# Optimization experiments

Measured on AMD Instinct MI355X. Metric: run time of the kernel, lower is better.

## Reference

```python
import jax, jax.numpy as jnp
import numpy as np

EPS = 1e-6
D = 512      # embedding_dim
M = 4        # n_modules
B = 4        # batch
S = 128      # seq_len
K = 32       # stack_size
STEPS = 16   # max_steps (ACT)
SCALE = D ** (-0.5)


def _clin(zr, zi, Wr, Wi, sub):
    # complex linear: (Wr + i Wi)(zr + i zi), torch Linear convention y = x @ W.T
    yr = jnp.einsum(sub, zr, Wr) - jnp.einsum(sub, zi, Wi)
    yi = jnp.einsum(sub, zi, Wr) + jnp.einsum(sub, zr, Wi)
    return yr, yi


def forward_fn(x_real, x_imag, Wl_r, Wl_i, Wq_r, Wq_i, Wk_r, Wk_i, Wv_r, Wv_i,
               ln_scale, ln_shift, mod_bias, gate_mask,
               score_w, score_b, conf_w, conf_b, halt_w, halt_b,
               ctrl_w, ctrl_b, st_score_w, st_score_b, st_conf_w, st_conf_b):
    mem0 = jnp.zeros((B, K, 2 * D), x_real.dtype)
    ptr0 = jnp.zeros((B, K), x_real.dtype).at[:, 0].set(1.0)
    acc0 = jnp.zeros((B, S, 2 * D), x_real.dtype)
    rem0 = jnp.ones((B,), x_real.dtype)

    def step(carry, _):
        sr, si, mem, ptr, acc, rem = carry
        # ComplexAttentionBlock (all M modules vectorized on axis m)
        cr = 0.5 * x_real + 0.5 * sr
        ci = 0.5 * x_imag + 0.5 * si
        zr, zi = _clin(cr, ci, Wl_r, Wl_i, 'bsd,mod->bmso')   # [B,M,S,D]
        # ComplexLayerNorm (magnitude LN, unbiased var as torch.var default)
        mag = jnp.sqrt(zr * zr + zi * zi) + EPS
        mean = mag.mean(-1, keepdims=True)
        var = mag.var(-1, keepdims=True, ddof=1)
        nm = (mag - mean) / jnp.sqrt(var + EPS)
        nm = nm * ln_scale[None, :, None, :] + ln_shift[None, :, None, :]
        ph = jnp.arctan2(zi, zr)
        zr = nm * jnp.cos(ph)
        zi = nm * jnp.sin(ph)
        # ModReLU
        nrm = jnp.sqrt(zr * zr + zi * zi) + EPS
        sc = jax.nn.relu(nrm + mod_bias[None, :, None, :]) / nrm
        zr = zr * sc
        zi = zi * sc
        # ComplexAttention over concatenated real/imag q,k
        sub = 'bmsd,mod->bmso'
        qr, qi = _clin(zr, zi, Wq_r, Wq_i, sub)
        kr, ki = _clin(zr, zi, Wk_r, Wk_i, sub)
        vr, vi = _clin(zr, zi, Wv_r, Wv_i, sub)
        qf = jnp.concatenate([qr, qi], -1)   # [B,M,S,2D]
        kf = jnp.concatenate([kr, ki], -1)
        attn = jax.nn.softmax(jnp.einsum('bmse,bmte->bmst', qf, kf) * SCALE, axis=-1)
        ar = jnp.einsum('bmst,bmtd->bmsd', attn, vr)
        ai = jnp.einsum('bmst,bmtd->bmsd', attn, vi)
        # SigmoidGatingMask
        g = jax.nn.sigmoid(gate_mask)[None, :, None, :]
        pr = ar * g
        pi = ai * g
        flat = jnp.concatenate([pr, pi], -1)  # [B,M,S,2D]
        score = jnp.einsum('bmse,me->bms', flat, score_w) + score_b[None, :, None]
        conf = jax.nn.sigmoid(jnp.einsum('bmse,me->bms', flat, conf_w) + conf_b[None, :, None])
        halt = jnp.einsum('bmse,me->bms', flat, halt_w) + halt_b[None, :, None]
        # DifferentiableStack on seq-pooled broadcast state
        flat_in = jnp.concatenate([sr.mean(1), si.mean(1)], -1)  # [B,2D]
        control = jax.nn.softmax(flat_in @ ctrl_w + ctrl_b, axis=-1)  # [B,3]
        push, pop, noop = control[:, 0:1], control[:, 1:2], control[:, 2:3]
        ptr_up = jnp.roll(ptr, 1, axis=1)
        ptr_dn = jnp.roll(ptr, -1, axis=1)
        new_ptr = push * ptr_up + pop * ptr_dn + noop * ptr
        new_ptr = new_ptr / (new_ptr.sum(1, keepdims=True) + EPS)
        wmask = push * ptr_up                                   # [B,K]
        new_mem = wmask[..., None] * flat_in[:, None, :] + mem * (1.0 - wmask[..., None])
        read = (new_mem * new_ptr[..., None]).sum(1)            # [B,2D]
        sp_r, sp_i = read[:, :D], read[:, D:]
        st_sc = read @ st_score_w + st_score_b[0]               # [B]
        st_cf = jax.nn.sigmoid(read @ st_conf_w + st_conf_b[0])
        # combine M block proposals + stack proposal via score*confidence softmax
        all_pr = jnp.concatenate([pr, jnp.broadcast_to(sp_r[:, None, None, :], (B, 1, S, D))], 1)
        all_pi = jnp.concatenate([pi, jnp.broadcast_to(sp_i[:, None, None, :], (B, 1, S, D))], 1)
        all_sc = jnp.concatenate([score, jnp.broadcast_to(st_sc[:, None, None], (B, 1, S))], 1)
        all_cf = jnp.concatenate([conf, jnp.broadcast_to(st_cf[:, None, None], (B, 1, S))], 1)
        w = jax.nn.softmax(all_sc * all_cf, axis=1)[..., None]  # [B,M+1,S,1]
        new_sr = (w * all_pr).sum(1)
        new_si = (w * all_pi).sum(1)
        # ACT halting accumulation
        p = jax.nn.sigmoid(halt).mean(axis=(1, 2))              # [B]
        acc = acc + (p * rem)[:, None, None] * jnp.concatenate([new_sr, new_si], -1)
        rem = rem * (1.0 - p)
        return (new_sr, new_si, new_mem, new_ptr, acc, rem), None

    carry, _ = jax.lax.scan(step, (x_real, x_imag, mem0, ptr0, acc0, rem0), None, length=STEPS)
    sr, si, _, _, acc, rem = carry
    # add ACT remainder weight on final state
    out = acc + rem[:, None, None] * jnp.concatenate([sr, si], -1)
    return out  # [B,S,2D] real/imag concat


def setup_inputs() -> dict:
    key = jax.random.key(0)
    ks = jax.random.split(key, 24)
    w = 1.0 / np.sqrt(D)
    h = 0.02
    inp = {
        'x_real': jax.random.normal(ks[0], (B, S, D), jnp.float32),
        'x_imag': jax.random.normal(ks[1], (B, S, D), jnp.float32),
        'Wl_r': jax.random.normal(ks[2], (M, D, D), jnp.float32) * w,
        'Wl_i': jax.random.normal(ks[3], (M, D, D), jnp.float32) * w,
        'Wq_r': jax.random.normal(ks[4], (M, D, D), jnp.float32) * w,
        'Wq_i': jax.random.normal(ks[5], (M, D, D), jnp.float32) * w,
        'Wk_r': jax.random.normal(ks[6], (M, D, D), jnp.float32) * w,
        'Wk_i': jax.random.normal(ks[7], (M, D, D), jnp.float32) * w,
        'Wv_r': jax.random.normal(ks[8], (M, D, D), jnp.float32) * w,
        'Wv_i': jax.random.normal(ks[9], (M, D, D), jnp.float32) * w,
        'ln_scale': jnp.ones((M, D), jnp.float32),
        'ln_shift': jnp.zeros((M, D), jnp.float32),
        'mod_bias': jnp.zeros((M, D), jnp.float32),
        'gate_mask': jnp.ones((M, D), jnp.float32),
        'score_w': jax.random.normal(ks[10], (M, 2 * D), jnp.float32) * h,
        'score_b': jnp.zeros((M,), jnp.float32),
        'conf_w': jax.random.normal(ks[11], (M, 2 * D), jnp.float32) * h,
        'conf_b': jnp.zeros((M,), jnp.float32),
        'halt_w': jax.random.normal(ks[12], (M, 2 * D), jnp.float32) * h,
        'halt_b': jnp.full((M,), -4.0, jnp.float32),  # nn.init.constant_(halt_head.bias, -4.0)
        'ctrl_w': jax.random.normal(ks[13], (2 * D, 3), jnp.float32) * h,
        'ctrl_b': jnp.zeros((3,), jnp.float32),
        'st_score_w': jax.random.normal(ks[14], (2 * D,), jnp.float32) * h,
        'st_score_b': jnp.zeros((1,), jnp.float32),
        'st_conf_w': jax.random.normal(ks[15], (2 * D,), jnp.float32) * h,
        'st_conf_b': jnp.zeros((1,), jnp.float32),
    }
    return inp


def reference(x_real, x_imag, Wl_r, Wl_i, Wq_r, Wq_i, Wk_r, Wk_i, Wv_r, Wv_i,
              ln_scale, ln_shift, mod_bias, gate_mask,
              score_w, score_b, conf_w, conf_b, halt_w, halt_b,
              ctrl_w, ctrl_b, st_score_w, st_score_b, st_conf_w, st_conf_b):
    return forward_fn(x_real, x_imag, Wl_r, Wl_i, Wq_r, Wq_i, Wk_r, Wk_i, Wv_r, Wv_i,
                      ln_scale, ln_shift, mod_bias, gate_mask,
                      score_w, score_b, conf_w, conf_b, halt_w, halt_b,
                      ctrl_w, ctrl_b, st_score_w, st_score_b, st_conf_w, st_conf_b)
```

## Files before the change

kernel.cpp:

```cpp
#include <hip/hip_runtime.h>

#define DD 512
#define MM 4
#define BB 4
#define SS 128
#define KK 32
#define NSTEPS 16
#define EPSF 1e-6f
#define SCALEF 0.04419417382415922f
#define BMSD (BB * MM * SS * DD)

typedef unsigned short u16;
typedef __bf16 bf16x8 __attribute__((ext_vector_type(8)));
typedef u16 u16x8 __attribute__((ext_vector_type(8)));
typedef float f32x16 __attribute__((ext_vector_type(16)));
typedef unsigned int u32x4 __attribute__((ext_vector_type(4)));

__device__ inline void split_bf16(float x, u16& h, u16& l) {
  __bf16 hb = (__bf16)x;
  float hf = (float)hb;
  __bf16 lb = (__bf16)(x - hf);
  h = __builtin_bit_cast(u16, hb);
  l = __builtin_bit_cast(u16, lb);
}
// ... 156 lines not shown
  int l31 = lane & 31, khalf = (lane >> 5) * 8;

  f32x16 accP, accN, accI;
  for (int i = 0; i < 16; i++) { accP[i] = 0.f; accN[i] = 0.f; accI[i] = 0.f; }

  int it20 = split;
  int seg0 = it20 >> 3, k00 = (it20 & 7) * 64;
  int aofs0 = (seg0 == 1) ? 512 : 0, wofs0 = (seg0 == 2) ? 512 : 0;
  u16x8 g0 = *(const u16x8*)&Ar[arow0 * 1024 + aofs0 + k00 + lk8];
  u16x8 g1 = *(const u16x8*)&Ar[arow1 * 1024 + aofs0 + k00 + lk8];
  u16x8 g2 = *(const u16x8*)&Ai[arow0 * 1024 + aofs0 + k00 + lk8];
  u16x8 g3 = *(const u16x8*)&Ai[arow1 * 1024 + aofs0 + k00 + lk8];
  u16x8 g4 = *(const u16x8*)&Wr[wrow0 * 1024 + wofs0 + k00 + lk8];
  u16x8 g5 = *(const u16x8*)&Wr[wrow1 * 1024 + wofs0 + k00 + lk8];
  u16x8 g6 = *(const u16x8*)&Wi[wrow0 * 1024 + wofs0 + k00 + lk8];
  u16x8 g7 = *(const u16x8*)&Wi[wrow1 * 1024 + wofs0 + k00 + lk8];

  for (int jt = 0; jt < 12; ++jt) {
    __syncthreads();
    *(u16x8*)&sAr[lrow][lk8] = g0;
    *(u16x8*)&sAr[lrow + 32][lk8] = g1;
    *(u16x8*)&sAi[lrow][lk8] = g2;
    *(u16x8*)&sAi[lrow + 32][lk8] = g3;
    *(u16x8*)&sWr[lrow][lk8] = g4;
    *(u16x8*)&sWr[lrow + 32][lk8] = g5;
    *(u16x8*)&sWi[lrow][lk8] = g6;
    *(u16x8*)&sWi[lrow + 32][lk8] = g7;
    u16x8 n0, n1, n2, n3, n4, n5, n6, n7;
    if (jt < 11) {
      int it2 = 2 * (jt + 1) + split, seg = it2 >> 3, k0 = (it2 & 7) * 64;
      int aofs = (seg == 1) ? 512 : 0, wofs = (seg == 2) ? 512 : 0;
      n0 = *(const u16x8*)&Ar[arow0 * 1024 + aofs + k0 + lk8];
      n1 = *(const u16x8*)&Ar[arow1 * 1024 + aofs + k0 + lk8];
      n2 = *(const u16x8*)&Ai[arow0 * 1024 + aofs + k0 + lk8];
      n3 = *(const u16x8*)&Ai[arow1 * 1024 + aofs + k0 + lk8];
      n4 = *(const u16x8*)&Wr[wrow0 * 1024 + wofs + k0 + lk8];
      n5 = *(const u16x8*)&Wr[wrow1 * 1024 + wofs + k0 + lk8];
      n6 = *(const u16x8*)&Wi[wrow0 * 1024 + wofs + k0 + lk8];
      n7 = *(const u16x8*)&Wi[wrow1 * 1024 + wofs + k0 + lk8];
    }
    __syncthreads();
#pragma unroll
    for (int kk = 0; kk < 64; kk += 16) {
      bf16x8 fAr = *(const bf16x8*)&sAr[wrow + l31][kk + khalf];
      bf16x8 fAi = *(const bf16x8*)&sAi[wrow + l31][kk + khalf];
      bf16x8 fWr = *(const bf16x8*)&sWr[wcol + l31][kk + khalf];
      bf16x8 fWi = *(const bf16x8*)&sWi[wcol + l31][kk + khalf];
      accP = __builtin_amdgcn_mfma_f32_32x32x16_bf16(fAr, fWr, accP, 0, 0, 0);
      accN = __builtin_amdgcn_mfma_f32_32x32x16_bf16(fAi, fWi, accN, 0, 0, 0);
      accI = __builtin_amdgcn_mfma_f32_32x32x16_bf16(fAi, fWr, accI, 0, 0, 0);
      accI = __builtin_amdgcn_mfma_f32_32x32x16_bf16(fAr, fWi, accI, 0, 0, 0);
    }
    if (jt < 11) {
      g0 = n0; g1 = n1; g2 = n2; g3 = n3; g4 = n4; g5 = n5; g6 = n6; g7 = n7;
    }
  }

  int o = o_blk + wcol + l31;
  size_t sofs = (size_t)split * BMSD;
#pragma unroll
  for (int reg = 0; reg < 16; reg++) {
    int r_in = (reg & 3) + 8 * (reg >> 2) + 4 * (lane >> 5);
    int gr = row_blk + wrow + r_in;
    int b = gr >> 7, s = gr & (SS - 1);
    size_t crow = (size_t)((b * MM + m) * SS + s);
    Cr[sofs + crow * DD + o] = accP[reg] - accN[reg];
    Ci[sofs + crow * DD + o] = accI[reg];
  }
}

__global__ __launch_bounds__(256) void k_gemm_g(
    const u16* __restrict__ Ar, const u16* __restrict__ Ai,
    const u16* __restrict__ Wr, const u16* __restrict__ Wi,
    float* __restrict__ Hr, float* __restrict__ Hi) {
  __shared__ u16 sAr[64][LSTR], sAi[64][LSTR], sWr[64][LSTR], sWi[64][LSTR];
  int m = blockIdx.z;
  int row_blk = blockIdx.y * 64, o_blk = blockIdx.x * 64;
  int tid = threadIdx.x;

  int lrow = tid >> 3, lk8 = (tid & 7) << 3;
  size_t arow0 = (size_t)(m * 512 + row_blk + lrow), arow1 = arow0 + 32;
  size_t wrow0 = (size_t)(m * 512 + o_blk + lrow), wrow1 = wrow0 + 32;

  int wave = tid >> 6, lane = tid & 63;
  int wrow = (wave >> 1) * 32, wcol = (wave & 1) * 32;
  int l31 = lane & 31, khalf = (lane >> 5) * 8;

  f32x16 accP, accN, accI;
  for (int i = 0; i < 16; i++) { accP[i] = 0.f; accN[i] = 0.f; accI[i] = 0.f; }

  u16x8 g0 = *(const u16x8*)&Ar[arow0 * 1024 + lk8];
  u16x8 g1 = *(const u16x8*)&Ar[arow1 * 1024 + lk8];
  u16x8 g2 = *(const u16x8*)&Ai[arow0 * 1024 + lk8];
  u16x8 g3 = *(const u16x8*)&Ai[arow1 * 1024 + lk8];
  u16x8 g4 = *(const u16x8*)&Wr[wrow0 * 1024 + lk8];
  u16x8 g5 = *(const u16x8*)&Wr[wrow1 * 1024 + lk8];
  u16x8 g6 = *(const u16x8*)&Wi[wrow0 * 1024 + lk8];
  u16x8 g7 = *(const u16x8*)&Wi[wrow1 * 1024 + lk8];

  for (int it = 0; it < 24; ++it) {
    __syncthreads();
    *(u16x8*)&sAr[lrow][lk8] = g0;
    *(u16x8*)&sAr[lrow + 32][lk8] = g1;
    *(u16x8*)&sAi[lrow][lk8] = g2;
    *(u16x8*)&sAi[lrow + 32][lk8] = g3;
    *(u16x8*)&sWr[lrow][lk8] = g4;
    *(u16x8*)&sWr[lrow + 32][lk8] = g5;
    *(u16x8*)&sWi[lrow][lk8] = g6;
    *(u16x8*)&sWi[lrow + 32][lk8] = g7;
    u16x8 n0, n1, n2, n3, n4, n5, n6, n7;
    if (it < 23) {
      int it2 = it + 1, seg = it2 >> 3, k0 = (it2 & 7) * 64;
      int aofs = (seg == 1) ? 512 : 0, wofs = (seg == 2) ? 512 : 0;
      n0 = *(const u16x8*)&Ar[arow0 * 1024 + aofs + k0 + lk8];
      n1 = *(const u16x8*)&Ar[arow1 * 1024 + aofs + k0 + lk8];
      n2 = *(const u16x8*)&Ai[arow0 * 1024 + aofs + k0 + lk8];
      n3 = *(const u16x8*)&Ai[arow1 * 1024 + aofs + k0 + lk8];
      n4 = *(const u16x8*)&Wr[wrow0 * 1024 + wofs + k0 + lk8];
      n5 = *(const u16x8*)&Wr[wrow1 * 1024 + wofs + k0 + lk8];
      n6 = *(const u16x8*)&Wi[wrow0 * 1024 + wofs + k0 + lk8];
      n7 = *(const u16x8*)&Wi[wrow1 * 1024 + wofs + k0 + lk8];
    }
    __syncthreads();
#pragma unroll
    for (int kk = 0; kk < 64; kk += 16) {
      bf16x8 fAr = *(const bf16x8*)&sAr[wrow + l31][kk + khalf];
      bf16x8 fAi = *(const bf16x8*)&sAi[wrow + l31][kk + khalf];
      bf16x8 fWr = *(const bf16x8*)&sWr[wcol + l31][kk + khalf];
      bf16x8 fWi = *(const bf16x8*)&sWi[wcol + l31][kk + khalf];
      u32x4 t = __builtin_bit_cast(u32x4, fAi) ^ 0x80008000u;
      bf16x8 nAi = __builtin_bit_cast(bf16x8, t);
      accP = __builtin_amdgcn_mfma_f32_32x32x16_bf16(fAr, fWr, accP, 0, 0, 0);
      accN = __builtin_amdgcn_mfma_f32_32x32x16_bf16(fAi, fWi, accN, 0, 0, 0);
      accI = __builtin_amdgcn_mfma_f32_32x32x16_bf16(fAr, fWi, accI, 0, 0, 0);
      accI = __builtin_amdgcn_mfma_f32_32x32x16_bf16(nAi, fWr, accI, 0, 0, 0);
    }
    if (it < 23) {
      g0 = n0; g1 = n1; g2 = n2; g3 = n3; g4 = n4; g5 = n5; g6 = n6; g7 = n7;
    }
  }

  int o = o_blk + wcol + l31;
#pragma unroll
  for (int reg = 0; reg < 16; reg++) {
    int r_in = (reg & 3) + 8 * (reg >> 2) + 4 * (lane >> 5);
    int gr = row_blk + wrow + r_in;
    size_t crow = (size_t)(m * 512 + gr);
    Hr[crow * DD + o] = accP[reg] + accN[reg];
    Hi[crow * DD + o] = accI[reg];
  }
}

__global__ __launch_bounds__(256) void k_gemm_qkv(
    const u16* __restrict__ Ar, const u16* __restrict__ Ai,
    const u16* __restrict__ wbf, size_t WSLOT,
    u16* __restrict__ qbr, u16* __restrict__ qbi,
    u16* __restrict__ vbr, u16* __restrict__ vbi) {
  __shared__ u16 sAr[64][LSTR], sAi[64][LSTR], sWr[64][LSTR], sWi[64][LSTR];
  int zid = blockIdx.x;
  int m = zid >> 1, w = zid & 1;
  int slot = (w == 0) ? 8 : 6;
  const u16* Wr = wbf + (size_t)slot * WSLOT;
  const u16* Wi = Wr + WSLOT;
  int row_blk = blockIdx.z * 64, o_blk = blockIdx.y * 64;
  int tid = threadIdx.x;

  int lrow = tid >> 3, lk8 = (tid & 7) << 3;
  int gr0 = row_blk + lrow, gr1 = gr0 + 32;
  size_t arow0 = (size_t)(((gr0 >> 7) * MM + m) * SS + (gr0 & (SS - 1)));
  size_t arow1 = (size_t)(((gr1 >> 7) * MM + m) * SS + (gr1 & (SS - 1)));
  size_t wrow0 = (size_t)m * DD + o_blk + lrow, wrow1 = wrow0 + 32;

  int wave = tid >> 6, lane = tid & 63;
  int wrow = (wave >> 1) * 32, wcol = (wave & 1) * 32;
  int l31 = lane & 31, khalf = (lane >> 5) * 8;

  f32x16 accP, accN, accI;
  for (int i = 0; i < 16; i++) { accP[i] = 0.f; accN[i] = 0.f; accI[i] = 0.f; }

  u16x8 g0 = *(const u16x8*)&Ar[arow0 * 1024 + lk8];
  u16x8 g1 = *(const u16x8*)&Ar[arow1 * 1024 + lk8];
  u16x8 g2 = *(const u16x8*)&Ai[arow0 * 1024 + lk8];
  u16x8 g3 = *(const u16x8*)&Ai[arow1 * 1024 + lk8];
  u16x8 g4 = *(const u16x8*)&Wr[wrow0 * 1024 + lk8];
  u16x8 g5 = *(const u16x8*)&Wr[wrow1 * 1024 + lk8];
  u16x8 g6 = *(const u16x8*)&Wi[wrow0 * 1024 + lk8];
  u16x8 g7 = *(const u16x8*)&Wi[wrow1 * 1024 + lk8];

  for (int it = 0; it < 24; ++it) {
    __syncthreads();
    *(u16x8*)&sAr[lrow][lk8] = g0;
    *(u16x8*)&sAr[lrow + 32][lk8] = g1;
    *(u16x8*)&sAi[lrow][lk8] = g2;
    *(u16x8*)&sAi[lrow + 32][lk8] = g3;
    *(u16x8*)&sWr[lrow][lk8] = g4;
    *(u16x8*)&sWr[lrow + 32][lk8] = g5;
    *(u16x8*)&sWi[lrow][lk8] = g6;
    *(u16x8*)&sWi[lrow + 32][lk8] = g7;
    u16x8 n0, n1, n2, n3, n4, n5, n6, n7;
    if (it < 23) {
      int it2 = it + 1, seg = it2 >> 3, k0 = (it2 & 7) * 64;
      int aofs = (seg == 1) ? 512 : 0, wofs = (seg == 2) ? 512 : 0;
      n0 = *(const u16x8*)&Ar[arow0 * 1024 + aofs + k0 + lk8];
      n1 = *(const u16x8*)&Ar[arow1 * 1024 + aofs + k0 + lk8];
      n2 = *(const u16x8*)&Ai[arow0 * 1024 + aofs + k0 + lk8];
      n3 = *(const u16x8*)&Ai[arow1 * 1024 + aofs + k0 + lk8];
      n4 = *(const u16x8*)&Wr[wrow0 * 1024 + wofs + k0 + lk8];
      n5 = *(const u16x8*)&Wr[wrow1 * 1024 + wofs + k0 + lk8];
      n6 = *(const u16x8*)&Wi[wrow0 * 1024 + wofs + k0 + lk8];
      n7 = *(const u16x8*)&Wi[wrow1 * 1024 + wofs + k0 + lk8];
    }
    __syncthreads();
#pragma unroll
    for (int kk = 0; kk < 64; kk += 16) {
      bf16x8 fAr = *(const bf16x8*)&sAr[wrow + l31][kk + khalf];
      bf16x8 fAi = *(const bf16x8*)&sAi[wrow + l31][kk + khalf];
      bf16x8 fWr = *(const bf16x8*)&sWr[wcol + l31][kk + khalf];
      bf16x8 fWi = *(const bf16x8*)&sWi[wcol + l31][kk + khalf];
      accP = __builtin_amdgcn_mfma_f32_32x32x16_bf16(fAr, fWr, accP, 0, 0, 0);
      accN = __builtin_amdgcn_mfma_f32_32x32x16_bf16(fAi, fWi, accN, 0, 0, 0);
      accI = __builtin_amdgcn_mfma_f32_32x32x16_bf16(fAi, fWr, accI, 0, 0, 0);
      accI = __builtin_amdgcn_mfma_f32_32x32x16_bf16(fAr, fWi, accI, 0, 0, 0);
    }
    if (it < 23) {
      g0 = n0; g1 = n1; g2 = n2; g3 = n3; g4 = n4; g5 = n5; g6 = n6; g7 = n7;
    }
  }

  u16* Cr = (w == 0) ? qbr : vbr;
  u16* Ci = (w == 0) ? qbi : vbi;
  int o = o_blk + wcol + l31;
#pragma unroll
  for (int reg = 0; reg < 16; reg++) {
    int r_in = (reg & 3) + 8 * (reg >> 2) + 4 * (lane >> 5);
    int gr = row_blk + wrow + r_in;
    int b = gr >> 7, s = gr & (SS - 1);
    size_t crow = (size_t)((b * MM + m) * SS + s);
    u16 h, l;
    split_bf16(accP[reg] - accN[reg], h, l);
    Cr[crow * 1024 + o] = h;
    Cr[crow * 1024 + 512 + o] = l;
    split_bf16(accI[reg], h, l);
    Ci[crow * 1024 + o] = h;
    Ci[crow * 1024 + 512 + o] = l;
  }
}

__global__ __launch_bounds__(256) void k_scores_sm(
    const u16* __restrict__ Q_r, const u16* __restrict__ Q_i,
    const u16* __restrict__ K_r, const u16* __restrict__ K_i,
    u16* __restrict__ Pb) {
  __shared__ __align__(16) char smem[55296];
  u16 (*sQr)[LSTR] = (u16(*)[LSTR])smem;
  u16 (*sQi)[LSTR] = (u16(*)[LSTR])(smem + 9216);
  u16 (*sKr)[LSTR] = (u16(*)[LSTR])(smem + 18432);
  u16 (*sKi)[LSTR] = (u16(*)[LSTR])(smem + 36864);
  float (*stile)[132] = (float(*)[132])smem;

  int bm = blockIdx.z;
  int s_blk = blockIdx.y * 64;
  int tid = threadIdx.x;
  int lrow = tid >> 3, lk8 = (tid & 7) << 3;
  size_t qrow0 = (size_t)(bm * SS + s_blk + lrow), qrow1 = qrow0 + 32;
  size_t krow = (size_t)(bm * SS + lrow);

  int wave = tid >> 6, lane = tid & 63;
  int srow_w = (wave & 1) * 32;
  int tcol_w = (wave >> 1) * 64;
  int l31 = lane & 31, khalf = (lane >> 5) * 8;

  f32x16 acc0, acc1;
  for (int i = 0; i < 16; i++) { acc0[i] = 0.f; acc1[i] = 0.f; }

  u16x8 pf[12];
  pf[0] = *(const u16x8*)&Q_r[qrow0 * 1024 + lk8];
  pf[1] = *(const u16x8*)&Q_r[qrow1 * 1024 + lk8];
  pf[2] = *(const u16x8*)&Q_i[qrow0 * 1024 + lk8];
  pf[3] = *(const u16x8*)&Q_i[qrow1 * 1024 + lk8];
#pragma unroll
  for (int q = 0; q < 4; q++) {
    pf[4 + q] = *(const u16x8*)&K_r[(krow + q * 32) * 1024 + lk8];
    pf[8 + q] = *(const u16x8*)&K_i[(krow + q * 32) * 1024 + lk8];
  }

  for (int it = 0; it < 24; ++it) {
    __syncthreads();
    *(u16x8*)&sQr[lrow][lk8] = pf[0];
    *(u16x8*)&sQr[lrow + 32][lk8] = pf[1];
    *(u16x8*)&sQi[lrow][lk8] = pf[2];
    *(u16x8*)&sQi[lrow + 32][lk8] = pf[3];
#pragma unroll
    for (int q = 0; q < 4; q++) {
      *(u16x8*)&sKr[lrow + q * 32][lk8] = pf[4 + q];
      *(u16x8*)&sKi[lrow + q * 32][lk8] = pf[8 + q];
    }
    u16x8 nf[12];
    if (it < 23) {
      int it2 = it + 1, seg = it2 >> 3, k0 = (it2 & 7) * 64;
      int qofs = (seg == 1) ? 512 : 0;
      int kofs = (seg == 2) ? 512 : 0;
      nf[0] = *(const u16x8*)&Q_r[qrow0 * 1024 + qofs + k0 + lk8];
      nf[1] = *(const u16x8*)&Q_r[qrow1 * 1024 + qofs + k0 + lk8];
      nf[2] = *(const u16x8*)&Q_i[qrow0 * 1024 + qofs + k0 + lk8];
      nf[3] = *(const u16x8*)&Q_i[qrow1 * 1024 + qofs + k0 + lk8];
#pragma unroll
      for (int q = 0; q < 4; q++) {
        nf[4 + q] = *(const u16x8*)&K_r[(krow + q * 32) * 1024 + kofs + k0 + lk8];
        nf[8 + q] = *(const u16x8*)&K_i[(krow + q * 32) * 1024 + kofs + k0 + lk8];
      }
    }
    __syncthreads();
#pragma unroll
    for (int kk = 0; kk < 64; kk += 16) {
      bf16x8 fQr = *(const bf16x8*)&sQr[srow_w + l31][kk + khalf];
      bf16x8 fQi = *(const bf16x8*)&sQi[srow_w + l31][kk + khalf];
      bf16x8 fKr0 = *(const bf16x8*)&sKr[tcol_w + l31][kk + khalf];
      bf16x8 fKr1 = *(const bf16x8*)&sKr[tcol_w + 32 + l31][kk + khalf];
      bf16x8 fKi0 = *(const bf16x8*)&sKi[tcol_w + l31][kk + khalf];
      bf16x8 fKi1 = *(const bf16x8*)&sKi[tcol_w + 32 + l31][kk + khalf];
      acc0 = __builtin_amdgcn_mfma_f32_32x32x16_bf16(fQr, fKr0, acc0, 0, 0, 0);
      acc0 = __builtin_amdgcn_mfma_f32_32x32x16_bf16(fQi, fKi0, acc0, 0, 0, 0);
      acc1 = __builtin_amdgcn_mfma_f32_32x32x16_bf16(fQr, fKr1, acc1, 0, 0, 0);
      acc1 = __builtin_amdgcn_mfma_f32_32x32x16_bf16(fQi, fKi1, acc1, 0, 0, 0);
    }
    if (it < 23) {
#pragma unroll
      for (int j = 0; j < 12; j++) pf[j] = nf[j];
    }
  }

  __syncthreads();
#pragma unroll
  for (int reg = 0; reg < 16; reg++) {
    int r = srow_w + (reg & 3) + 8 * (reg >> 2) + 4 * (lane >> 5);
    stile[r][tcol_w + l31] = acc0[reg] * SCALEF;
    stile[r][tcol_w + 32 + l31] = acc1[reg] * SCALEF;
  }
  __syncthreads();
  int row = tid >> 2;
  int quarter = tid & 3;
  float mx = -3.4e38f;
#pragma unroll
  for (int j = 0; j < 32; j++) mx = fmaxf(mx, stile[row][quarter * 32 + j]);
  mx = fmaxf(mx, __shfl_xor(mx, 1));
  mx = fmaxf(mx, __shfl_xor(mx, 2));
  float ev[32];
  float sum = 0.f;
#pragma unroll
  for (int j = 0; j < 32; j++) {
    ev[j] = expf(stile[row][quarter * 32 + j] - mx);
    sum += ev[j];
  }
  sum += __shfl_xor(sum, 1);
  sum += __shfl_xor(sum, 2);
  float inv = 1.f / sum;
  size_t prow = (size_t)(bm * SS + s_blk + row) * 256;
#pragma unroll
  for (int j = 0; j < 32; j++) {
    int c = quarter * 32 + j;
    u16 h, l;
    split_bf16(ev[j] * inv, h, l);
    Pb[prow + c] = h;
    Pb[prow + 128 + c] = l;
  }
}

__global__ __launch_bounds__(256) void k_pv(
    const u16* __restrict__ Pb, const u16* __restrict__ vbr, const u16* __restrict__ vbi,
    const float* __restrict__ gate_mask,
    const float* __restrict__ score_w, const float* __restrict__ conf_w,
    const float* __restrict__ halt_w,
    float* __restrict__ pr, float* __restrict__ pi,
    float* __restrict__ scorev, float* __restrict__ confv, float* __restrict__ haltv) {
  __shared__ u16 sP[64][LSTR], sVr[64][LSTR], sVi[64][LSTR];
  int bm = blockIdx.z;
  int m = bm & (MM - 1);
  int s_blk = blockIdx.y * 64;
  int o_blk = blockIdx.x * 64;
  int tid = threadIdx.x;
  int lrow = tid >> 3, lk8 = (tid & 7) << 3;
  size_t prow0 = (size_t)(bm * SS + s_blk + lrow), prow1 = prow0 + 32;

  int wave = tid >> 6, lane = tid & 63;
  int wrow = (wave >> 1) * 32;
  int wcol = (wave & 1) * 32;
  int l31 = lane & 31, khalf = (lane >> 5) * 8;

  f32x16 accR, accI;
  for (int i = 0; i < 16; i++) { accR[i] = 0.f; accI[i] = 0.f; }

  for (int it = 0; it < 6; ++it) {
    int seg = it >> 1, k0 = (it & 1) * 64;
    int pofs = (seg == 1) ? 128 : 0;
    int vofs = (seg == 2) ? 512 : 0;
    u16x8 p0 = *(const u16x8*)&Pb[prow0 * 256 + pofs + k0 + lk8];
    u16x8 p1 = *(const u16x8*)&Pb[prow1 * 256 + pofs + k0 + lk8];
    size_t vrow0 = (size_t)(bm * SS + k0 + lrow), vrow1 = vrow0 + 32;
    u16x8 v0 = *(const u16x8*)&vbr[vrow0 * 1024 + vofs + o_blk + lk8];
    u16x8 v1 = *(const u16x8*)&vbr[vrow1 * 1024 + vofs + o_blk + lk8];
    u16x8 w0 = *(const u16x8*)&vbi[vrow0 * 1024 + vofs + o_blk + lk8];
    u16x8 w1 = *(const u16x8*)&vbi[vrow1 * 1024 + vofs + o_blk + lk8];
    __syncthreads();
    *(u16x8*)&sP[lrow][lk8] = p0;
    *(u16x8*)&sP[lrow + 32][lk8] = p1;
    *(u16x8*)&sVr[lrow][lk8] = v0;
    *(u16x8*)&sVr[lrow + 32][lk8] = v1;
    *(u16x8*)&sVi[lrow][lk8] = w0;
    *(u16x8*)&sVi[lrow + 32][lk8] = w1;
    __syncthreads();
#pragma unroll
    for (int kk = 0; kk < 64; kk += 16) {
      bf16x8 fP = *(const bf16x8*)&sP[wrow + l31][kk + khalf];
      u16x8 ar, ai;
#pragma unroll
      for (int j = 0; j < 8; j++) {
        ar[j] = sVr[kk + khalf + j][wcol + l31];
        ai[j] = sVi[kk + khalf + j][wcol + l31];
      }
      accR = __builtin_amdgcn_mfma_f32_32x32x16_bf16(fP, __builtin_bit_cast(bf16x8, ar), accR, 0, 0, 0);
      accI = __builtin_amdgcn_mfma_f32_32x32x16_bf16(fP, __builtin_bit_cast(bf16x8, ai), accI, 0, 0, 0);
    }
  }

  int d = o_blk + wcol + l31;
  float g = 1.f / (1.f + expf(-gate_mask[m * DD + d]));
  float swr = score_w[m * 2 * DD + d], swi = score_w[m * 2 * DD + DD + d];
  float cwr = conf_w[m * 2 * DD + d],  cwi = conf_w[m * 2 * DD + DD + d];
  float hwr = halt_w[m * 2 * DD + d],  hwi = halt_w[m * 2 * DD + DD + d];
#pragma unroll
  for (int reg = 0; reg < 16; reg++) {
    int r_in = (reg & 3) + 8 * (reg >> 2) + 4 * (lane >> 5);
    size_t crow = (size_t)(bm * SS + s_blk + wrow + r_in);
    float vR = accR[reg] * g, vI = accI[reg] * g;
    pr[crow * DD + d] = vR;
    pi[crow * DD + d] = vI;
    float ps = vR * swr + vI * swi;
    float pc = vR * cwr + vI * cwi;
    float ph = vR * hwr + vI * hwi;
#pragma unroll
    for (int off = 1; off < 32; off <<= 1) {
      ps += __shfl_xor(ps, off);
      pc += __shfl_xor(pc, off);
      ph += __shfl_xor(ph, off);
    }
    if (l31 == 0) {
      atomicAdd(&scorev[crow], ps);
      atomicAdd(&confv[crow], pc);
      atomicAdd(&haltv[crow], ph);
    }
  }
}

__global__ void k_lnphase(const float* __restrict__ zr, const float* __restrict__ zi,
                          const float* __restrict__ ln_scale, const float* __restrict__ ln_shift,
                          const float* __restrict__ mod_bias,
                          u16* __restrict__ zbr, u16* __restrict__ zbi) {
  int row = blockIdx.x;
  int m = (row >> 7) & (MM - 1);
  int tid = threadIdx.x;
  size_t base = (size_t)row * DD;
  float zrv[4], ziv[4], rv[4];
  float sum = 0.f, sumsq = 0.f;
#pragma unroll
  for (int i = 0; i < 4; i++) {
    int o = tid + i * 128;
    float a = zr[base + o] + zr[(size_t)BMSD + base + o];
    float bv = zi[base + o] + zi[(size_t)BMSD + base + o];
    zrv[i] = a; ziv[i] = bv;
    float r = sqrtf(a * a + bv * bv);
    rv[i] = r;
    float mg = r + EPSF;
    sum += mg;
    sumsq += mg * mg;
  }
  __shared__ float rs[128], rq[128];
  rs[tid] = sum; rq[tid] = sumsq;
  __syncthreads();
  for (int off = 64; off > 0; off >>= 1) {
    if (tid < off) { rs[tid] += rs[tid + off]; rq[tid] += rq[tid + off]; }
    __syncthreads();
  }
  float mean = rs[0] * (1.0f / DD);
  float var = (rq[0] - (float)DD * mean * mean) * (1.0f / (DD - 1));
  float inv = 1.0f / sqrtf(var + EPSF);
#pragma unroll
  for (int i = 0; i < 4; i++) {
    int o = tid + i * 128;
    float mg = rv[i] + EPSF;
    float nm = (mg - mean) * inv * ln_scale[m * DD + o] + ln_shift[m * DD + o];
    float r = rv[i];
    float cosp, sinp;
    if (r > 0.f) { cosp = zrv[i] / r; sinp = ziv[i] / r; }
    else { cosp = 1.f; sinp = 0.f; }
    float z1r = nm * cosp, z1i = nm * sinp;
    float nrm = sqrtf(z1r * z1r + z1i * z1i) + EPSF;
    float sc = fmaxf(nrm + mod_bias[m * DD + o], 0.f) / nrm;
    u16 h, l;
    split_bf16(z1r * sc, h, l);
    zbr[(size_t)row * 1024 + o] = h;
    zbr[(size_t)row * 1024 + 512 + o] = l;
    split_bf16(z1i * sc, h, l);
    zbi[(size_t)row * 1024 + o] = h;
    zbi[(size_t)row * 1024 + 512 + o] = l;
  }
}

__global__ void k_memup(const float* __restrict__ flat_in,
                        const float* __restrict__ nptrg, const float* __restrict__ wmg,
                        float* __restrict__ memv, float* __restrict__ readv,
                        const float* __restrict__ st_score_w, const float* __restrict__ st_conf_w,
                        float* __restrict__ stacc) {
  int b = blockIdx.x >> 2;
  int chunk = blockIdx.x & 3;
  int tid = threadIdx.x;
  int e = chunk * 256 + tid;
  __shared__ float nptr[KK], wm[KK];
  __shared__ float red[256], red2[256];
  if (tid < KK) { nptr[tid] = nptrg[b * KK + tid]; wm[tid] = wmg[b * KK + tid]; }
  __syncthreads();
  float fl = flat_in[b * 2 * DD + e];
  float racc = 0.f;
#pragma unroll
  for (int k = 0; k < KK; k++) {
    size_t idx = ((size_t)(b * KK + k)) * 2 * DD + e;
    float nm = wm[k] * fl + memv[idx] * (1.f - wm[k]);
    memv[idx] = nm;
    racc += nm * nptr[k];
  }
  readv[b * 2 * DD + e] = racc;
  red[tid] = racc * st_score_w[e];
  red2[tid] = racc * st_conf_w[e];
  __syncthreads();
  for (int off = 128; off > 0; off >>= 1) {
    if (tid < off) { red[tid] += red[tid + off]; red2[tid] += red2[tid + off]; }
    __syncthreads();
  }
  if (tid == 0) {
    atomicAdd(&stacc[b * 2], red[0]);
    atomicAdd(&stacc[b * 2 + 1], red2[0]);
  }
}

__global__ void k_haltp(const float* __restrict__ halt, const float* __restrict__ halt_b,
                        float* __restrict__ rem,
                        float* __restrict__ coeff, const float* __restrict__ stacc,
                        const float* __restrict__ st_score_b, const float* __restrict__ st_conf_b,
                        float* __restrict__ stv) {
  int b = blockIdx.x;
  int tid = threadIdx.x;
  __shared__ float red[256];
  float v0 = halt[b * MM * SS + tid] + halt_b[tid >> 7];
  float v1 = halt[b * MM * SS + 256 + tid] + halt_b[(tid + 256) >> 7];
  red[tid] = 1.f / (1.f + expf(-v0)) + 1.f / (1.f + expf(-v1));
  __syncthreads();
  for (int off = 128; off > 0; off >>= 1) {
    if (tid < off) red[tid] += red[tid + off];
    __syncthreads();
  }
  if (tid == 0) {
    float p = red[0] * (1.0f / (MM * SS));
    float r = rem[b];
    coeff[b] = p * r;
    rem[b] = r * (1.f - p);
    stv[b] = stacc[b * 2] + st_score_b[0];
    stv[BB + b] = 1.f / (1.f + expf(-(stacc[b * 2 + 1] + st_conf_b[0])));
  }
}

__global__ void k_combine(const float* __restrict__ pr, const float* __restrict__ pi,
                          const float* __restrict__ score, const float* __restrict__ conf,
                          const float* __restrict__ score_b, const float* __restrict__ conf_b,
                          const float* __restrict__ stv, const float* __restrict__ readv,
                          const float* __restrict__ coeff,
                          const float* __restrict__ xr, const float* __restrict__ xi,
                          float* __restrict__ sr, float* __restrict__ si, float* __restrict__ acc,
                          u16* __restrict__ crbf, u16* __restrict__ cibf) {
  int bs = blockIdx.x;
  int b = bs >> 7, s = bs & (SS - 1);
  int tid = threadIdx.x;
  __shared__ float w[5];
  if (tid == 0) {
    float l[5];
    for (int m = 0; m < MM; m++) {
      int r = (b * MM + m) * SS + s;
      float sc = score[r] + score_b[m];
      float cf = 1.f / (1.f + expf(-(conf[r] + conf_b[m])));
      l[m] = sc * cf;
    }
    l[4] = stv[b] * stv[BB + b];
    float mx = l[0];
    for (int j = 1; j < 5; j++) mx = fmaxf(mx, l[j]);
    float sum = 0.f;
    for (int j = 0; j < 5; j++) { l[j] = expf(l[j] - mx); sum += l[j]; }
    for (int j = 0; j < 5; j++) w[j] = l[j] / sum;
  }
  __syncthreads();
  float cf = coeff[b];
#pragma unroll
  for (int i = 0; i < 2; i++) {
    int d = tid + i * 256;
    float nsr = w[4] * readv[b * 2 * DD + d];
    float nsi = w[4] * readv[b * 2 * DD + DD + d];
#pragma unroll
    for (int m = 0; m < MM; m++) {
      size_t off = ((size_t)((b * MM + m) * SS + s)) * DD + d;
      nsr += w[m] * pr[off];
      nsi += w[m] * pi[off];
    }
    size_t sidx = (size_t)bs * DD + d;
    sr[sidx] = nsr;
    si[sidx] = nsi;
    size_t aoff = (size_t)bs * 2 * DD;
    acc[aoff + d] += cf * nsr;
    acc[aoff + DD + d] += cf * nsi;
    u16 h, l;
    split_bf16(0.5f * xr[sidx] + 0.5f * nsr, h, l);
    crbf[(size_t)bs * 1024 + d] = h;
    crbf[(size_t)bs * 1024 + 512 + d] = l;
    split_bf16(0.5f * xi[sidx] + 0.5f * nsi, h, l);
    cibf[(size_t)bs * 1024 + d] = h;
    cibf[(size_t)bs * 1024 + 512 + d] = l;
  }
}

__global__ void k_final(const float* __restrict__ acc, const float* __restrict__ rem,
                        const float* __restrict__ sr, const float* __restrict__ si,
                        float* __restrict__ out) {
  int idx = blockIdx.x * 256 + threadIdx.x;
  int e = idx & (2 * DD - 1);
  int bs = idx >> 10;
  int b = bs >> 7;
  float v = (e < DD) ? sr[(size_t)bs * DD + e] : si[(size_t)bs * DD + e - DD];
  out[idx] = acc[idx] + rem[b] * v;
}

extern "C" void kernel_launch(void* const* d_in, const int* in_sizes, int n_in,
                              void* d_out, int out_size, void* d_ws, size_t ws_size,
                              hipStream_t stream) {
  const float* xr = (const float*)d_in[0];
  const float* xi = (const float*)d_in[1];
  const float* Wl_r = (const float*)d_in[2];
  const float* Wl_i = (const float*)d_in[3];
  const float* Wq_r = (const float*)d_in[4];
  const float* Wq_i = (const float*)d_in[5];
  const float* Wk_r = (const float*)d_in[6];
  const float* Wk_i = (const float*)d_in[7];
  const float* Wv_r = (const float*)d_in[8];
  const float* Wv_i = (const float*)d_in[9];
  const float* ln_scale = (const float*)d_in[10];
  const float* ln_shift = (const float*)d_in[11];
  const float* mod_bias = (const float*)d_in[12];
  const float* gate_mask = (const float*)d_in[13];
  const float* score_w = (const float*)d_in[14];
  const float* score_b = (const float*)d_in[15];
  const float* conf_w = (const float*)d_in[16];
  const float* conf_b = (const float*)d_in[17];
  const float* halt_w = (const float*)d_in[18];
  const float* halt_b = (const float*)d_in[19];
  const float* ctrl_w = (const float*)d_in[20];
  const float* ctrl_b = (const float*)d_in[21];
  const float* st_score_w = (const float*)d_in[22];
  const float* st_score_b = (const float*)d_in[23];
  const float* st_conf_w = (const float*)d_in[24];
  const float* st_conf_b = (const float*)d_in[25];
  float* out = (float*)d_out;

  const int BSD = BB * SS * DD;
  const size_t WSLOT = (size_t)MM * DD * 1024;

  char* pc = (char*)d_ws;
  float* sr = (float*)pc; pc += (size_t)BSD * 4;
  float* si = (float*)pc; pc += (size_t)BSD * 4;
  float* zr = (float*)pc; pc += (size_t)2 * BMSD * 4;
  float* zi = (float*)pc; pc += (size_t)2 * BMSD * 4;
  float* prb = (float*)pc; pc += (size_t)BMSD * 4;
  float* pib = (float*)pc; pc += (size_t)BMSD * 4;
  float* scorev = (float*)pc; pc += (size_t)BB * MM * SS * 4;
  float* confv = (float*)pc; pc += (size_t)BB * MM * SS * 4;
  float* haltv = (float*)pc; pc += (size_t)BB * MM * SS * 4;
  float* flat = (float*)pc; pc += (size_t)BB * 2 * DD * 4;
  float* stacc = (float*)pc; pc += 64;
  float* nptrg = (float*)pc; pc += (size_t)BB * KK * 4;
  float* wmg = (float*)pc; pc += (size_t)BB * KK * 4;
  float* memv = (float*)pc; pc += (size_t)BB * KK * 2 * DD * 4;
  float* ptrv = (float*)pc; pc += (size_t)BB * KK * 4;
  float* readv = (float*)pc; pc += (size_t)BB * 2 * DD * 4;
  float* stv = (float*)pc; pc += (size_t)2 * BB * 4;
  float* accb = (float*)pc; pc += (size_t)BB * SS * 2 * DD * 4;
  float* rem = (float*)pc; pc += (size_t)BB * 4;
  float* coeff = (float*)pc; pc += (size_t)BB * 4;
  u16* crbf = (u16*)pc; pc += (size_t)BB * SS * 1024 * 2;
  u16* cibf = (u16*)pc; pc += (size_t)BB * SS * 1024 * 2;
  u16* zbr = (u16*)pc; pc += (size_t)BB * MM * SS * 1024 * 2;
  u16* zbi = (u16*)pc; pc += (size_t)BB * MM * SS * 1024 * 2;
  u16* qbr = (u16*)pc; pc += (size_t)BB * MM * SS * 1024 * 2;
  u16* qbi = (u16*)pc; pc += (size_t)BB * MM * SS * 1024 * 2;
  u16* vbr = (u16*)pc; pc += (size_t)BB * MM * SS * 1024 * 2;
  u16* vbi = (u16*)pc; pc += (size_t)BB * MM * SS * 1024 * 2;
  u16* Pb  = (u16*)pc; pc += (size_t)BB * MM * SS * 256 * 2;
  u16* wbf = (u16*)pc; pc += 10 * WSLOT * 2;
  u16* wqtr = (u16*)pc; pc += WSLOT * 2;
  u16* wqti = (u16*)pc; pc += WSLOT * 2;
  u16* wktr = (u16*)pc; pc += WSLOT * 2;
  u16* wkti = (u16*)pc; pc += WSLOT * 2;
  float* hfr = (float*)pc; pc += (size_t)MM * DD * DD * 4;
  float* hfi = (float*)pc; pc += (size_t)MM * DD * DD * 4;

  k_convw<<<4096, 256, 0, stream>>>(Wl_r, wbf + 0 * WSLOT);
  k_convw<<<4096, 256, 0, stream>>>(Wl_i, wbf + 1 * WSLOT);
  k_convw<<<4096, 256, 0, stream>>>(Wv_r, wbf + 6 * WSLOT);
  k_convw<<<4096, 256, 0, stream>>>(Wv_i, wbf + 7 * WSLOT);

  dim3 tgrid(8, 8, 4);
  k_convt<<<tgrid, 256, 0, stream>>>(Wq_r, wqtr);
  k_convt<<<tgrid, 256, 0, stream>>>(Wq_i, wqti);
  k_convt<<<tgrid, 256, 0, stream>>>(Wk_r, wktr);
  k_convt<<<tgrid, 256, 0, stream>>>(Wk_i, wkti);

  dim3 hgrid(8, 8, 4);
  k_gemm_g<<<hgrid, 256, 0, stream>>>(wktr, wkti, wqtr, wqti, hfr, hfi);
  k_convw<<<4096, 256, 0, stream>>>(hfr, wbf + 8 * WSLOT);
  k_convw<<<4096, 256, 0, stream>>>(hfi, wbf + 9 * WSLOT);

  k_init<<<2048, 256, 0, stream>>>(xr, xi, sr, si, accb, memv, ptrv, rem, crbf, cibf);

  dim3 ggrid(DD / 64, (BB * SS) / 64, MM * 2);
  dim3 qgrid(MM * 2, DD / 64, (BB * SS) / 64);
  dim3 smgrid(1, SS / 64, BB * MM);
  dim3 pvgrid(DD / 64, SS / 64, BB * MM);

  for (int step = 0; step < NSTEPS; ++step) {
    k_flatctrl<<<BB, 256, 0, stream>>>(sr, si, ctrl_w, ctrl_b, ptrv, flat, nptrg, wmg, stacc,
                                       scorev, confv, haltv);
    k_gemm_mfma<<<ggrid, 256, 0, stream>>>(crbf, cibf, wbf + 0 * WSLOT, wbf + 1 * WSLOT, zr, zi);
    k_lnphase<<<BB * MM * SS, 128, 0, stream>>>(zr, zi, ln_scale, ln_shift, mod_bias, zbr, zbi);
    k_gemm_qkv<<<qgrid, 256, 0, stream>>>(zbr, zbi, wbf, WSLOT, qbr, qbi, vbr, vbi);
    k_scores_sm<<<smgrid, 256, 0, stream>>>(qbr, qbi, zbr, zbi, Pb);
    k_pv<<<pvgrid, 256, 0, stream>>>(Pb, vbr, vbi, gate_mask, score_w, conf_w, halt_w,
                                     prb, pib, scorev, confv, haltv);
    k_memup<<<BB * 4, 256, 0, stream>>>(flat, nptrg, wmg, memv, readv,
                                        st_score_w, st_conf_w, stacc);
    k_haltp<<<BB, 256, 0, stream>>>(haltv, halt_b, rem, coeff, stacc, st_score_b, st_conf_b, stv);
    k_combine<<<BB * SS, 256, 0, stream>>>(prb, pib, scorev, confv, score_b, conf_b,
                                           stv, readv, coeff,
                                           xr, xi, sr, si, accb, crbf, cibf);
  }

  k_final<<<(BB * SS * 2 * DD) / 256, 256, 0, stream>>>(accb, rem, sr, si, out);
}
```

Measured before the change: 2.121 ms.

## Store V transposed from QKV GEMM so PV kernel reads contiguous MFMA fragments

The V projection inside the QKV GEMM now computes the transposed product by swapping operands (weights as A, activations as B) and writes V in a [b,m,d,s] layout with hi/lo bf16 halves along s. The PV kernel then loads V rows along the sequence dimension and reads MFMA B fragments with single vector LDS loads, replacing the per-element strided gather from shared memory. This removes LDS bank-conflicting scalar reads in PV, at the cost of narrower, strided global stores in the V epilogue.

```diff
diff --git a/kernel.cpp b/kernel.cpp
--- a/kernel.cpp
+++ b/kernel.cpp
@@ -332,40 +332,49 @@
 }
 
 __global__ __launch_bounds__(256) void k_gemm_qkv(
-    const u16* __restrict__ Ar, const u16* __restrict__ Ai,
+    const u16* __restrict__ Az_r, const u16* __restrict__ Az_i,
     const u16* __restrict__ wbf, size_t WSLOT,
     u16* __restrict__ qbr, u16* __restrict__ qbi,
-    u16* __restrict__ vbr, u16* __restrict__ vbi) {
+    u16* __restrict__ vbtr, u16* __restrict__ vbti) {
   __shared__ u16 sAr[64][LSTR], sAi[64][LSTR], sWr[64][LSTR], sWi[64][LSTR];
   int zid = blockIdx.x;
   int m = zid >> 1, w = zid & 1;
-  int slot = (w == 0) ? 8 : 6;
-  const u16* Wr = wbf + (size_t)slot * WSLOT;
-  const u16* Wi = Wr + WSLOT;
-  int row_blk = blockIdx.z * 64, o_blk = blockIdx.y * 64;
-  int tid = threadIdx.x;
-
+  int tid = threadIdx.x;
   int lrow = tid >> 3, lk8 = (tid & 7) << 3;
-  int gr0 = row_blk + lrow, gr1 = gr0 + 32;
-  size_t arow0 = (size_t)(((gr0 >> 7) * MM + m) * SS + (gr0 & (SS - 1)));
-  size_t arow1 = (size_t)(((gr1 >> 7) * MM + m) * SS + (gr1 & (SS - 1)));
-  size_t wrow0 = (size_t)m * DD + o_blk + lrow, wrow1 = wrow0 + 32;
-
   int wave = tid >> 6, lane = tid & 63;
   int wrow = (wave >> 1) * 32, wcol = (wave & 1) * 32;
   int l31 = lane & 31, khalf = (lane >> 5) * 8;
 
+  const u16 *Ar, *Ai, *Wr, *Wi;
+  size_t ra0, ra1, rw0, rw1;
+  if (w == 0) {
+    Ar = Az_r; Ai = Az_i;
+    Wr = wbf + (size_t)8 * WSLOT; Wi = wbf + (size_t)9 * WSLOT;
+    int row_blk = blockIdx.z * 64, o_blk = blockIdx.y * 64;
+    int gr0 = row_blk + lrow, gr1 = gr0 + 32;
+    ra0 = (size_t)(((gr0 >> 7) * MM + m) * SS + (gr0 & (SS - 1)));
+    ra1 = (size_t)(((gr1 >> 7) * MM + m) * SS + (gr1 & (SS - 1)));
+    rw0 = (size_t)m * DD + o_blk + lrow; rw1 = rw0 + 32;
+  } else {
+    Ar = wbf + (size_t)6 * WSLOT; Ai = wbf + (size_t)7 * WSLOT;
+    Wr = Az_r; Wi = Az_i;
+    int d_blk = blockIdx.y * 64;
+    int b = blockIdx.z >> 1, s0 = (blockIdx.z & 1) * 64;
+    ra0 = (size_t)m * DD + d_blk + lrow; ra1 = ra0 + 32;
+    rw0 = (size_t)((b * MM + m) * SS) + s0 + lrow; rw1 = rw0 + 32;
+  }
+
   f32x16 accP, accN, accI;
   for (int i = 0; i < 16; i++) { accP[i] = 0.f; accN[i] = 0.f; accI[i] = 0.f; }
 
-  u16x8 g0 = *(const u16x8*)&Ar[arow0 * 1024 + lk8];
-  u16x8 g1 = *(const u16x8*)&Ar[arow1 * 1024 + lk8];
-  u16x8 g2 = *(const u16x8*)&Ai[arow0 * 1024 + lk8];
-  u16x8 g3 = *(const u16x8*)&Ai[arow1 * 1024 + lk8];
-  u16x8 g4 = *(const u16x8*)&Wr[wrow0 * 1024 + lk8];
-  u16x8 g5 = *(const u16x8*)&Wr[wrow1 * 1024 + lk8];
-  u16x8 g6 = *(const u16x8*)&Wi[wrow0 * 1024 + lk8];
-  u16x8 g7 = *(const u16x8*)&Wi[wrow1 * 1024 + lk8];
+  u16x8 g0 = *(const u16x8*)&Ar[ra0 * 1024 + lk8];
+  u16x8 g1 = *(const u16x8*)&Ar[ra1 * 1024 + lk8];
+  u16x8 g2 = *(const u16x8*)&Ai[ra0 * 1024 + lk8];
+  u16x8 g3 = *(const u16x8*)&Ai[ra1 * 1024 + lk8];
+  u16x8 g4 = *(const u16x8*)&Wr[rw0 * 1024 + lk8];
+  u16x8 g5 = *(const u16x8*)&Wr[rw1 * 1024 + lk8];
+  u16x8 g6 = *(const u16x8*)&Wi[rw0 * 1024 + lk8];
+  u16x8 g7 = *(const u16x8*)&Wi[rw1 * 1024 + lk8];
 
   for (int it = 0; it < 24; ++it) {
     __syncthreads();
@@ -381,14 +390,14 @@
     if (it < 23) {
       int it2 = it + 1, seg = it2 >> 3, k0 = (it2 & 7) * 64;
       int aofs = (seg == 1) ? 512 : 0, wofs = (seg == 2) ? 512 : 0;
-      n0 = *(const u16x8*)&Ar[arow0 * 1024 + aofs + k0 + lk8];
-      n1 = *(const u16x8*)&Ar[arow1 * 1024 + aofs + k0 + lk8];
-      n2 = *(const u16x8*)&Ai[arow0 * 1024 + aofs + k0 + lk8];
-      n3 = *(const u16x8*)&Ai[arow1 * 1024 + aofs + k0 + lk8];
-      n4 = *(const u16x8*)&Wr[wrow0 * 1024 + wofs + k0 + lk8];
-      n5 = *(const u16x8*)&Wr[wrow1 * 1024 + wofs + k0 + lk8];
-      n6 = *(const u16x8*)&Wi[wrow0 * 1024 + wofs + k0 + lk8];
-      n7 = *(const u16x8*)&Wi[wrow1 * 1024 + wofs + k0 + lk8];
+      n0 = *(const u16x8*)&Ar[ra0 * 1024 + aofs + k0 + lk8];
+      n1 = *(const u16x8*)&Ar[ra1 * 1024 + aofs + k0 + lk8];
+      n2 = *(const u16x8*)&Ai[ra0 * 1024 + aofs + k0 + lk8];
+      n3 = *(const u16x8*)&Ai[ra1 * 1024 + aofs + k0 + lk8];
+      n4 = *(const u16x8*)&Wr[rw0 * 1024 + wofs + k0 + lk8];
+      n5 = *(const u16x8*)&Wr[rw1 * 1024 + wofs + k0 + lk8];
+      n6 = *(const u16x8*)&Wi[rw0 * 1024 + wofs + k0 + lk8];
+      n7 = *(const u16x8*)&Wi[rw1 * 1024 + wofs + k0 + lk8];
     }
     __syncthreads();
 #pragma unroll
@@ -407,22 +416,38 @@
     }
   }
 
-  u16* Cr = (w == 0) ? qbr : vbr;
-  u16* Ci = (w == 0) ? qbi : vbi;
-  int o = o_blk + wcol + l31;
-#pragma unroll
-  for (int reg = 0; reg < 16; reg++) {
-    int r_in = (reg & 3) + 8 * (reg >> 2) + 4 * (lane >> 5);
-    int gr = row_blk + wrow + r_in;
-    int b = gr >> 7, s = gr & (SS - 1);
-    size_t crow = (size_t)((b * MM + m) * SS + s);
-    u16 h, l;
-    split_bf16(accP[reg] - accN[reg], h, l);
-    Cr[crow * 1024 + o] = h;
-    Cr[crow * 1024 + 512 + o] = l;
-    split_bf16(accI[reg], h, l);
-    Ci[crow * 1024 + o] = h;
-    Ci[crow * 1024 + 512 + o] = l;
+  if (w == 0) {
+    int o = blockIdx.y * 64 + wcol + l31;
+#pragma unroll
+    for (int reg = 0; reg < 16; reg++) {
+      int r_in = (reg & 3) + 8 * (reg >> 2) + 4 * (lane >> 5);
+      int gr = blockIdx.z * 64 + wrow + r_in;
+      int b = gr >> 7, s = gr & (SS - 1);
+      size_t crow = (size_t)((b * MM + m) * SS + s);
+      u16 h, l;
+      split_bf16(accP[reg] - accN[reg], h, l);
+      qbr[crow * 1024 + o] = h;
+      qbr[crow * 1024 + 512 + o] = l;
+      split_bf16(accI[reg], h, l);
+      qbi[crow * 1024 + o] = h;
+      qbi[crow * 1024 + 512 + o] = l;
+    }
+  } else {
+    int b = blockIdx.z >> 1;
+    int s = (blockIdx.z & 1) * 64 + wcol + l31;
+#pragma unroll
+    for (int reg = 0; reg < 16; reg++) {
+      int r_in = (reg & 3) + 8 * (reg >> 2) + 4 * (lane >> 5);
+      int d = blockIdx.y * 64 + wrow + r_in;
+      size_t crow = (size_t)((b * MM + m) * DD + d);
+      u16 h, l;
+      split_bf16(accP[reg] - accN[reg], h, l);
+      vbtr[crow * 256 + s] = h;
+      vbtr[crow * 256 + 128 + s] = l;
+      split_bf16(accI[reg], h, l);
+      vbti[crow * 256 + s] = h;
+      vbti[crow * 256 + 128 + s] = l;
+    }
   }
 }
 
@@ -546,7 +571,7 @@
 }
 
 __global__ __launch_bounds__(256) void k_pv(
-    const u16* __restrict__ Pb, const u16* __restrict__ vbr, const u16* __restrict__ vbi,
+    const u16* __restrict__ Pb, const u16* __restrict__ vbtr, const u16* __restrict__ vbti,
     const float* __restrict__ gate_mask,
     const float* __restrict__ score_w, const float* __restrict__ conf_w,
     const float* __restrict__ halt_w,
@@ -560,6 +585,7 @@
   int tid = threadIdx.x;
   int lrow = tid >> 3, lk8 = (tid & 7) << 3;
   size_t prow0 = (size_t)(bm * SS + s_blk + lrow), prow1 = prow0 + 32;
+  size_t vrow0 = (size_t)(bm * DD + o_blk + lrow), vrow1 = vrow0 + 32;
 
   int wave = tid >> 6, lane = tid & 63;
   int wrow = (wave >> 1) * 32;
@@ -572,14 +598,13 @@
   for (int it = 0; it < 6; ++it) {
     int seg = it >> 1, k0 = (it & 1) * 64;
     int pofs = (seg == 1) ? 128 : 0;
-    int vofs = (seg == 2) ? 512 : 0;
+    int vofs = (seg == 2) ? 128 : 0;
     u16x8 p0 = *(const u16x8*)&Pb[prow0 * 256 + pofs + k0 + lk8];
     u16x8 p1 = *(const u16x8*)&Pb[prow1 * 256 + pofs + k0 + lk8];
-    size_t vrow0 = (size_t)(bm * SS + k0 + lrow), vrow1 = vrow0 + 32;
-    u16x8 v0 = *(const u16x8*)&vbr[vrow0 * 1024 + vofs + o_blk + lk8];
-    u16x8 v1 = *(const u16x8*)&vbr[vrow1 * 1024 + vofs + o_blk + lk8];
-    u16x8 w0 = *(const u16x8*)&vbi[vrow0 * 1024 + vofs + o_blk + lk8];
-    u16x8 w1 = *(const u16x8*)&vbi[vrow1 * 1024 + vofs + o_blk + lk8];
+    u16x8 v0 = *(const u16x8*)&vbtr[vrow0 * 256 + vofs + k0 + lk8];
+    u16x8 v1 = *(const u16x8*)&vbtr[vrow1 * 256 + vofs + k0 + lk8];
+    u16x8 w0 = *(const u16x8*)&vbti[vrow0 * 256 + vofs + k0 + lk8];
+    u16x8 w1 = *(const u16x8*)&vbti[vrow1 * 256 + vofs + k0 + lk8];
     __syncthreads();
     *(u16x8*)&sP[lrow][lk8] = p0;
     *(u16x8*)&sP[lrow + 32][lk8] = p1;
@@ -591,14 +616,10 @@
 #pragma unroll
     for (int kk = 0; kk < 64; kk += 16) {
       bf16x8 fP = *(const bf16x8*)&sP[wrow + l31][kk + khalf];
-      u16x8 ar, ai;
-#pragma unroll
-      for (int j = 0; j < 8; j++) {
-        ar[j] = sVr[kk + khalf + j][wcol + l31];
-        ai[j] = sVi[kk + khalf + j][wcol + l31];
-      }
-      accR = __builtin_amdgcn_mfma_f32_32x32x16_bf16(fP, __builtin_bit_cast(bf16x8, ar), accR, 0, 0, 0);
-      accI = __builtin_amdgcn_mfma_f32_32x32x16_bf16(fP, __builtin_bit_cast(bf16x8, ai), accI, 0, 0, 0);
+      bf16x8 fVr = *(const bf16x8*)&sVr[wcol + l31][kk + khalf];
+      bf16x8 fVi = *(const bf16x8*)&sVi[wcol + l31][kk + khalf];
+      accR = __builtin_amdgcn_mfma_f32_32x32x16_bf16(fP, fVr, accR, 0, 0, 0);
+      accI = __builtin_amdgcn_mfma_f32_32x32x16_bf16(fP, fVi, accI, 0, 0, 0);
     }
   }
 
@@ -875,8 +896,8 @@
   u16* zbi = (u16*)pc; pc += (size_t)BB * MM * SS * 1024 * 2;
   u16* qbr = (u16*)pc; pc += (size_t)BB * MM * SS * 1024 * 2;
   u16* qbi = (u16*)pc; pc += (size_t)BB * MM * SS * 1024 * 2;
-  u16* vbr = (u16*)pc; pc += (size_t)BB * MM * SS * 1024 * 2;
-  u16* vbi = (u16*)pc; pc += (size_t)BB * MM * SS * 1024 * 2;
+  u16* vbtr = (u16*)pc; pc += (size_t)BB * MM * DD * 256 * 2;
+  u16* vbti = (u16*)pc; pc += (size_t)BB * MM * DD * 256 * 2;
   u16* Pb  = (u16*)pc; pc += (size_t)BB * MM * SS * 256 * 2;
   u16* wbf = (u16*)pc; pc += 10 * WSLOT * 2;
   u16* wqtr = (u16*)pc; pc += WSLOT * 2;
@@ -905,7 +926,7 @@
   k_init<<<2048, 256, 0, stream>>>(xr, xi, sr, si, accb, memv, ptrv, rem, crbf, cibf);
 
   dim3 ggrid(DD / 64, (BB * SS) / 64, MM * 2);
-  dim3 qgrid(MM * 2, DD / 64, (BB * SS) / 64);
+  dim3 qgrid(MM * 2, 8, 8);
   dim3 smgrid(1, SS / 64, BB * MM);
   dim3 pvgrid(DD / 64, SS / 64, BB * MM);
 
@@ -914,9 +935,9 @@
                                        scorev, confv, haltv);
     k_gemm_mfma<<<ggrid, 256, 0, stream>>>(crbf, cibf, wbf + 0 * WSLOT, wbf + 1 * WSLOT, zr, zi);
     k_lnphase<<<BB * MM * SS, 128, 0, stream>>>(zr, zi, ln_scale, ln_shift, mod_bias, zbr, zbi);
-    k_gemm_qkv<<<qgrid, 256, 0, stream>>>(zbr, zbi, wbf, WSLOT, qbr, qbi, vbr, vbi);
+    k_gemm_qkv<<<qgrid, 256, 0, stream>>>(zbr, zbi, wbf, WSLOT, qbr, qbi, vbtr, vbti);
     k_scores_sm<<<smgrid, 256, 0, stream>>>(qbr, qbi, zbr, zbi, Pb);
-    k_pv<<<pvgrid, 256, 0, stream>>>(Pb, vbr, vbi, gate_mask, score_w, conf_w, halt_w,
+    k_pv<<<pvgrid, 256, 0, stream>>>(Pb, vbtr, vbti, gate_mask, score_w, conf_w, halt_w,
                                      prb, pib, scorev, confv, haltv);
     k_memup<<<BB * 4, 256, 0, stream>>>(flat, nptrg, wmg, memv, readv,
                                         st_score_w, st_conf_w, stacc);
```

After: 2.113 ms, median of 2. No clear change (-0.4%).
